# Optimization experiments

Measured on AMD Instinct MI355X. Metric: run time of the kernel, lower is better.

The kernel has to match this reference:

```python
import jax, jax.numpy as jnp
import numpy as np

B, LI, LT, D, H, DH, E, I, IS, TOPK = 2, 1024, 256, 768, 12, 64, 8, 3072, 1536, 2


def _rms(x, s):
    # RMSNorm over last dim, eps=1e-6, learned scale s [DH]
    r = jax.lax.rsqrt(jnp.mean(x * x, axis=-1, keepdims=True) + 1e-6)
    return x * r * s


def _ln(x):
    # LayerNorm without affine (elementwise_affine=False), eps=1e-6
    m = jnp.mean(x, axis=-1, keepdims=True)
    v = jnp.mean((x - m) ** 2, axis=-1, keepdims=True)
    return (x - m) * jax.lax.rsqrt(v + 1e-6)


def _mlp(x, wg, wu, wd):
    # SwiGLU MoeMLP: down(silu(gate(x)) * up(x))
    return (jax.nn.silu(x @ wg.T) * (x @ wu.T)) @ wd.T


def _moe(x, gw, eg, eu, ed, sg, su, sd):
    # x: [T, D]. Softmax gate -> top-k (norm_topk_prob=False -> raw weights),
    # combine expert outputs weighted by routing probs, plus shared experts.
    scores = jax.nn.softmax(x @ gw.T, axis=-1)            # [T, E]
    tw, ti = jax.lax.top_k(scores, TOPK)                  # [T, K]
    T = x.shape[0]
    w = jnp.zeros((T, E), x.dtype).at[jnp.arange(T)[:, None], ti].add(tw)
    y = jnp.zeros_like(x)
    for e in range(E):  # fixed small expert count
        y = y + w[:, e:e + 1] * _mlp(x, eg[e], eu[e], ed[e])
    return y + _mlp(x, sg, su, sd)


def _mod(vec, w, b):
    # Modulation(double=True): Linear(silu(vec)) -> 6 chunks, broadcast over seq
    return jnp.split((jax.nn.silu(vec) @ w.T + b)[:, None, :], 6, axis=-1)


def _qkv(x, w, b, qs, ks):
    Bb, L, _ = x.shape
    qkv = (x @ w.T + b).reshape(Bb, L, 3, H, DH).transpose(2, 0, 3, 1, 4)  # [3,B,H,L,DH]
    q, k, v = qkv[0], qkv[1], qkv[2]
    return _rms(q, qs), _rms(k, ks), v


def _forward(img, txt, vec, imw, imb, tmw, tmb, iqkvw, iqkvb, ipw, ipb, tqkvw, tqkvb, tpw, tpb, iqs, iks, tqs, tks, igw, ieg, ieu, ied, isg, isu, isd, tgw, teg, teu, ted, tsg, tsu, tsd):
    is1, ic1, ig1, is2, ic2, ig2 = _mod(vec, imw, imb)
    ts1, tc1, tg1, ts2, tc2, tg2 = _mod(vec, tmw, tmb)
    iq, ik, iv = _qkv((1 + ic1) * _ln(img) + is1, iqkvw, iqkvb, iqs, iks)
    tq, tk, tv = _qkv((1 + tc1) * _ln(txt) + ts1, tqkvw, tqkvb, tqs, tks)
    # joint attention over concat(txt, img)
    q = jnp.concatenate([tq, iq], axis=2)
    k = jnp.concatenate([tk, ik], axis=2)
    v = jnp.concatenate([tv, iv], axis=2)
    a = jax.nn.softmax(jnp.einsum('bhqd,bhkd->bhqk', q, k) / np.float32(np.sqrt(DH)), axis=-1)
    o = jnp.einsum('bhqk,bhkd->bhqd', a, v).transpose(0, 2, 1, 3).reshape(B, LT + LI, D)
    txt_a, img_a = o[:, :LT], o[:, LT:]
    img = img + ig1 * (img_a @ ipw.T + ipb)
    txt = txt + tg1 * (txt_a @ tpw.T + tpb)
    img = img + ig2 * _moe(((1 + ic2) * _ln(img) + is2).reshape(-1, D), igw, ieg, ieu, ied, isg, isu, isd).reshape(B, LI, D)
    txt = txt + tg2 * _moe(((1 + tc2) * _ln(txt) + ts2).reshape(-1, D), tgw, teg, teu, ted, tsg, tsu, tsd).reshape(B, LT, D)
    return img, txt


def setup_inputs() -> dict:
    key = jax.random.key(0)
    ks = jax.random.split(key, 32)
    n = lambda i, sh, s=1.0: jax.random.normal(ks[i], sh, jnp.float32) * s
    W = 0.02
    return {
        'img': n(0, (B, LI, D)), 'txt': n(1, (B, LT, D)), 'vec': n(2, (B, D)),
        'imw': n(3, (6 * D, D), W), 'imb': n(4, (6 * D,), W),
        'tmw': n(5, (6 * D, D), W), 'tmb': n(6, (6 * D,), W),
        'iqkvw': n(7, (3 * D, D), W), 'iqkvb': n(8, (3 * D,), W),
        'ipw': n(9, (D, D), W), 'ipb': n(10, (D,), W),
        'tqkvw': n(11, (3 * D, D), W), 'tqkvb': n(12, (3 * D,), W),
        'tpw': n(13, (D, D), W), 'tpb': n(14, (D,), W),
        'iqs': jnp.ones((DH,), jnp.float32), 'iks': jnp.ones((DH,), jnp.float32),
        'tqs': jnp.ones((DH,), jnp.float32), 'tks': jnp.ones((DH,), jnp.float32),
        'igw': n(15, (E, D), W), 'ieg': n(16, (E, I, D), W), 'ieu': n(17, (E, I, D), W), 'ied': n(18, (E, D, I), W),
        'isg': n(19, (IS, D), W), 'isu': n(20, (IS, D), W), 'isd': n(21, (D, IS), W),
        'tgw': n(22, (E, D), W), 'teg': n(23, (E, I, D), W), 'teu': n(24, (E, I, D), W), 'ted': n(25, (E, D, I), W),
        'tsg': n(26, (IS, D), W), 'tsu': n(27, (IS, D), W), 'tsd': n(28, (D, IS), W),
    }


def reference(img, txt, vec, imw, imb, tmw, tmb, iqkvw, iqkvb, ipw, ipb, tqkvw, tqkvb, tpw, tpb, iqs, iks, tqs, tks, igw, ieg, ieu, ied, isg, isu, isd, tgw, teg, teu, ted, tsg, tsu, tsd):
    return _forward(img, txt, vec, imw, imb, tmw, tmb, iqkvw, iqkvb, ipw, ipb, tqkvw, tqkvb, tpw, tpb, iqs, iks, tqs, tks, igw, ieg, ieu, ied, isg, isu, isd, tgw, teg, teu, ted, tsg, tsu, tsd)
```

## Files before the change

kernel.cpp:

```cpp
#include <hip/hip_runtime.h>
#include <hip/hip_bf16.h>

using bf16 = __hip_bfloat16;
typedef __attribute__((ext_vector_type(4))) float f32x4;
typedef __attribute__((ext_vector_type(8))) short s16x8;

#define DEV static __device__ __forceinline__
DEV float bf2f(bf16 x){ return __bfloat162float(x); }
DEV bf16  f2bf(float x){ return __float2bfloat16(x); }
DEV float silu_(float x){ return x / (1.f + expf(-x)); }

template<bool B_F32, bool EXPERT, bool GATHER, int OUT, bool BIAS, bool PAIRB, bool MLOOP, bool ABLK>
DEV void gemm_core(
    const bf16* __restrict__ A,
    const void* __restrict__ B0a, const void* __restrict__ B0b,
    const void* __restrict__ B1a, const void* __restrict__ B1b,
    const float* __restrict__ bias, void* __restrict__ C,
    int M, int N, int K, int lda,
    long a_zoff, long b_zoff, int bshift, int biasz, int nsplitB,
    int zdiv, long c_so, long c_si, int ldc,
    float alpha, int ksplit, long c_spo,
    const int* __restrict__ rowlist, const int* __restrict__ offsets,
    const int* __restrict__ counts)
{
  __shared__ __align__(16) char smem_[36864];
  bf16 (*As)[72] = (bf16(*)[72])smem_;
  bf16 (*Bs)[72] = (bf16(*)[72])(smem_ + 18432);
  float (*st)[132] = (float(*)[132])smem_;

  const int zz = blockIdx.z;
  const int n0 = blockIdx.x * 128;
  const int z = zz / ksplit, split = zz % ksplit;
  int Meff = M; long rowbase = 0;
  if (EXPERT){ Meff = counts[z]; rowbase = offsets[z]; }
  int m0 = MLOOP ? 0 : blockIdx.y * 128;
  if (m0 >= Meff) return;
  const bf16* Ab = A + (EXPERT ? 0 : z * a_zoff);
  const int bidx = z >> bshift;
  const long e = (long)(z & ((1 << bshift) - 1));
  const void* BL = bidx ? B1a : B0a;
  const void* BU = bidx ? B1b : B0b;
  long coff;
  if (EXPERT) coff = rowbase * (long)ldc;
  else        coff = (long)(z / zdiv) * c_so + (long)(z % zdiv) * c_si;
  coff += (long)split * c_spo;
  const float* bias_eff = BIAS ? bias + (long)bidx * biasz : nullptr;

  const int klen = K / ksplit;
  const int kbeg = split * klen;
  const int NT = klen >> 6;

  const int tid = threadIdx.x;
  const int lane = tid & 63, wid = tid >> 6;
  const int wm = wid >> 1, wn = wid & 1;
  const int rbase = tid >> 3;
  const int kc = (tid & 7) << 3;

  const bf16* bp[4]; const float* bpf[4];
  bool bvalid[4];
  #pragma unroll
  for (int it = 0; it < 4; it++){
    int br = n0 + rbase + 32 * it;
    bvalid[it] = br < N;
    int brc = bvalid[it] ? br : 0;
    const void* Bsel; long brr;
    if (PAIRB){ Bsel = (brc & 1) ? BU : BL; brr = brc >> 1; }
    else { bool up = brc >= nsplitB; Bsel = up ? BU : BL; brr = up ? (brc - nsplitB) : brc; }
    if (B_F32) bpf[it] = (const float*)Bsel + e * b_zoff + brr * K + kbeg + kc;
    else       bp[it]  = (const bf16*) Bsel + e * b_zoff + brr * K + kbeg + kc;
  }

  const uint4 zero4 = make_uint4(0u,0u,0u,0u);
  const int er = tid >> 3;
  const int ec = (tid & 7) << 4;

  do {
    const bf16* ap[4];
    bool avalid[4];
    #pragma unroll
    for (int it = 0; it < 4; it++){
      int row = rbase + 32 * it;
      long ar = 0;
      if (EXPERT){
        int i = m0 + row;
        avalid[it] = i < Meff;
        if (avalid[it]) ar = GATHER ? (long)rowlist[rowbase + i] : (rowbase + i);
      } else {
        avalid[it] = (m0 + row) < Meff;
        ar = m0 + row;
      }
      if (ABLK) ap[it] = Ab + ((long)(kbeg >> 6) * lda + ar) * 64 + kc;
      else      ap[it] = Ab + ar * (long)lda + kbeg + kc;
    }

    uint4 ra[4], rb[4];
    float4 fb0[4], fb1[4];
    auto LOAD = [&](int koff){
      long aoff = ABLK ? (long)koff * lda : (long)koff;
      #pragma unroll
      for (int it = 0; it < 4; it++){
        ra[it] = avalid[it] ? *(const uint4*)(ap[it] + aoff) : zero4;
        if (B_F32){
          if (bvalid[it]){ fb0[it] = *(const float4*)(bpf[it] + koff);
                           fb1[it] = *(const float4*)(bpf[it] + koff + 4); }
          else { fb0[it] = make_float4(0,0,0,0); fb1[it] = make_float4(0,0,0,0); }
        } else {
          rb[it] = bvalid[it] ? *(const uint4*)(bp[it] + koff) : zero4;
        }
      }
    };
    auto STORE = [&](){
      #pragma unroll
      for (int it = 0; it < 4; it++){
        int row = rbase + 32 * it;
        *(uint4*)(&As[row][kc]) = ra[it];
        if (B_F32){
          union { bf16 h[8]; uint4 v; } u;
          u.h[0]=f2bf(fb0[it].x); u.h[1]=f2bf(fb0[it].y); u.h[2]=f2bf(fb0[it].z); u.h[3]=f2bf(fb0[it].w);
          u.h[4]=f2bf(fb1[it].x); u.h[5]=f2bf(fb1[it].y); u.h[6]=f2bf(fb1[it].z); u.h[7]=f2bf(fb1[it].w);
          *(uint4*)(&Bs[row][kc]) = u.v;
        } else {
          *(uint4*)(&Bs[row][kc]) = rb[it];
        }
      }
    };

    f32x4 acc[4][4] = {};
    LOAD(0);
    for (int t = 0; t < NT; t++){
      STORE();
      __syncthreads();
      if (t + 1 < NT) LOAD((t + 1) << 6);
      #pragma unroll
      for (int ks2 = 0; ks2 < 2; ks2++){
        const int r16 = lane & 15;
        const int kk = ks2 * 32 + ((lane >> 4) << 3);
        s16x8 af[4], bfr[4];
        #pragma unroll
        for (int mi = 0; mi < 4; mi++) af[mi]  = *(const s16x8*)(&As[wm*64 + mi*16 + r16][kk]);
        #pragma unroll
        for (int ni = 0; ni < 4; ni++) bfr[ni] = *(const s16x8*)(&Bs[wn*64 + ni*16 + r16][kk]);
        #pragma unroll
        for (int mi = 0; mi < 4; mi++)
          #pragma unroll
          for (int ni = 0; ni < 4; ni++)
            acc[mi][ni] = __builtin_amdgcn_mfma_f32_16x16x32_bf16(af[mi], bfr[ni], acc[mi][ni], 0, 0, 0);
      }
      __syncthreads();
    }

    const int erg = m0 + (er & 15) + ((er & 16) ? 64 : 0);
    #pragma unroll
    for (int mi = 0; mi < 4; mi++){
      #pragma unroll
      for (int ni = 0; ni < 4; ni++){
        int lc = wn*64 + ni*16 + (lane & 15);
        float bv = 0.f;
        if (BIAS){ if (split == 0) bv = bias_eff[n0 + lc]; }
        #pragma unroll
        for (int i = 0; i < 4; i++){
          int lr = wm*16 + ((lane >> 4) << 2) + i;
          st[lr][lc] = acc[mi][ni][i] * alpha + bv;
        }
      }
      __syncthreads();
      int rg = erg + mi*16;
      if (rg < Meff){
        if (OUT == 3){
          long base = ((long)(n0 >> 7) * (long)ldc + rowbase + rg) * 64 + (ec >> 1);
          union { bf16 h[8]; uint4 v; } o;
          #pragma unroll
          for (int j = 0; j < 8; j++)
            o.h[j] = f2bf(silu_(st[er][ec + 2*j]) * st[er][ec + 2*j + 1]);
          *(uint4*)((bf16*)C + base) = o.v;
        } else {
          int cg = n0 + ec;
          if (cg < N){
            long base = coff + (long)rg * ldc + cg;
            if (OUT == 0){
              float* dst = (float*)C + base;
              #pragma unroll
              for (int q = 0; q < 4; q++)
                *(float4*)(dst + 4*q) = make_float4(st[er][ec+4*q], st[er][ec+4*q+1],
                                                    st[er][ec+4*q+2], st[er][ec+4*q+3]);
            } else {
              union { bf16 h[8]; uint4 v; } o0, o1;
              #pragma unroll
              for (int j = 0; j < 8; j++){
                o0.h[j] = f2bf(st[er][ec+j]);
                o1.h[j] = f2bf(st[er][ec+8+j]);
              }
              *(uint4*)((bf16*)C + base)     = o0.v;
              *(uint4*)((bf16*)C + base + 8) = o1.v;
            }
          }
        }
      }
      __syncthreads();
    }
    m0 += 128;
  } while (MLOOP && m0 < Meff);
}

#define GEMM_K(NAME, BF32, EXPERT, GATHER, OUT, BIAS, PAIRB, MLOOP, ABLK)          \
__global__ __launch_bounds__(256) void NAME(                                       \
    const bf16* A, const void* B0a, const void* B0b, const void* B1a,              \
    const void* B1b, const float* bias, void* C,                                   \
    int M, int N, int K, int lda, long az, long bz, int bshift, int biasz,         \
    int nsplitB, int zdiv, long cso, long csi, int ldc, float alpha, int ks,       \
    long cspo, const int* rl, const int* ofs, const int* cnt){                     \
  gemm_core<BF32,EXPERT,GATHER,OUT,BIAS,PAIRB,MLOOP,ABLK>(A,B0a,B0b,B1a,B1b,bias,C,\
      M,N,K,lda,az,bz,bshift,biasz,nsplitB,zdiv,cso,csi,ldc,alpha,ks,cspo,rl,ofs,cnt); }

GEMM_K(k_qkv,  true ,true ,false,1,true ,false,false,false)
GEMM_K(k_qkt,  false,false,false,1,false,false,false,false)
GEMM_K(k_pv,   false,false,false,0,false,false,false,false)
GEMM_K(k_proj, true ,true ,false,0,true ,false,false,false)
GEMM_K(k_gup,  true ,true ,true ,3,false,true ,true ,false)
GEMM_K(k_down, true ,true ,false,1,false,false,true ,true )
GEMM_K(k_sgup, true ,true ,false,3,false,true ,false,false)
GEMM_K(k_sdown,true ,true ,false,0,false,false,false,true )

__global__ void init_kernel(int* cnt16, int* tabs){
  int i = threadIdx.x;
  if (i < 16) cnt16[i] = 0;
  if (i == 0){
    tabs[0]=2048; tabs[1]=512; tabs[2]=0; tabs[3]=2048;
    tabs[4]=256; tabs[5]=256; tabs[6]=1024; tabs[7]=1024;
    tabs[8]=0; tabs[9]=1280; tabs[10]=256; tabs[11]=1536;
    tabs[12]=2048; tabs[13]=512; tabs[14]=0; tabs[15]=2048;
  }
}
__global__ void tables_kernel(const int* cnt16, int* ofs16, int* cur16){
  if (threadIdx.x == 0){
    int o = 0;
    for (int e = 0; e < 8; e++){ ofs16[e] = o; o += cnt16[e]; cur16[e] = 0; }
    o = 4096;
    for (int e = 8; e < 16; e++){ ofs16[e] = o; o += cnt16[e]; cur16[e] = 0; }
  }
}

__global__ __launch_bounds__(256) void reduce_o_kernel(const float* __restrict__ Op,
    bf16* __restrict__ O, int chunk){
  int zh = blockIdx.y;
  int bh = chunk*12 + zh;
  int b = bh / 12, hh = bh % 12;
  int d = threadIdx.x & 63, rr = threadIdx.x >> 6;
  const float* base = Op + (long)zh * 1280 * 64;
  #pragma unroll
  for (int j = 0; j < 4; j++){
    int row = blockIdx.x * 16 + rr * 4 + j;
    float s = 0.f;
    #pragma unroll
    for (int sp = 0; sp < 5; sp++) s += base[(long)sp*12*1280*64 + (long)row*64 + d];
    O[((long)b*1280 + row)*768 + hh*64 + d] = f2bf(s);
  }
}

__global__ __launch_bounds__(256) void mod_kernel(const float* __restrict__ vec,
    const float* __restrict__ w, const float* __restrict__ b, float* __restrict__ out){
  int bb = blockIdx.y;
  __shared__ float sv[768];
  int tid = threadIdx.x;
  for (int i = tid; i < 768; i += 256){ float v = vec[bb*768 + i]; sv[i] = v/(1.f+expf(-v)); }
  __syncthreads();
  int w4 = tid >> 6, lane = tid & 63;
  int j0 = blockIdx.x * 8 + w4 * 2;
  for (int jj = 0; jj < 2; jj++){
    int j = j0 + jj;
    const float* wr = w + (long)j * 768;
    float p = 0.f;
    #pragma unroll
    for (int i = 0; i < 12; i++) p += sv[lane + 64*i] * wr[lane + 64*i];
    for (int o = 32; o; o >>= 1) p += __shfl_xor(p, o);
    if (lane == 0) out[bb*4608 + j] = p + b[j];
  }
}

__global__ __launch_bounds__(256) void ln_mod_kernel(const float* __restrict__ x,
    const float* __restrict__ mod, bf16* __restrict__ y, int L){
  int t = blockIdx.x; int b = t / L;
  const float* xr = x + (long)t * 768;
  __shared__ float red[256];
  int tid = threadIdx.x;
  float v[3]; float s = 0.f;
  #pragma unroll
  for (int i = 0; i < 3; i++){ v[i] = xr[tid + 256*i]; s += v[i]; }
  red[tid] = s; __syncthreads();
  for (int o = 128; o; o >>= 1){ if (tid < o) red[tid] += red[tid+o]; __syncthreads(); }
  float mean = red[0] * (1.f/768.f); __syncthreads();
  float s2 = 0.f;
  #pragma unroll
  for (int i = 0; i < 3; i++){ float d = v[i]-mean; s2 += d*d; }
  red[tid] = s2; __syncthreads();
  for (int o = 128; o; o >>= 1){ if (tid < o) red[tid] += red[tid+o]; __syncthreads(); }
  float rs = rsqrtf(red[0] * (1.f/768.f) + 1e-6f);
  const float* mb = mod + (long)b * 4608;
  #pragma unroll
  for (int i = 0; i < 3; i++){
    int d = tid + 256*i;
    y[(long)t*768 + d] = f2bf((1.f + mb[768+d]) * ((v[i]-mean)*rs) + mb[d]);
  }
}

__global__ __launch_bounds__(256) void resid_ln_mod_kernel(const float* __restrict__ x,
    const float* __restrict__ pj, int pjoff, long pjspo, const float* __restrict__ mod,
    float* __restrict__ h, bf16* __restrict__ y, float* __restrict__ yf, int L){
  int t = blockIdx.x; int b = t / L;
  const float* mb = mod + (long)b * 4608;
  const float* xr = x + (long)t * 768;
  long pr = (long)(pjoff + b*1280 + (t % L)) * 768;
  __shared__ float red[256];
  int tid = threadIdx.x;
  float v[3]; float s = 0.f;
  #pragma unroll
  for (int i = 0; i < 3; i++){
    int d = tid + 256*i;
    float pv = pj[pr + d] + pj[pjspo + pr + d];
    float hv = xr[d] + mb[2*768 + d] * pv;
    h[(long)t*768 + d] = hv;
    v[i] = hv; s += hv;
  }
  red[tid] = s; __syncthreads();
  for (int o = 128; o; o >>= 1){ if (tid < o) red[tid] += red[tid+o]; __syncthreads(); }
  float mean = red[0] * (1.f/768.f); __syncthreads();
  float s2 = 0.f;
  #pragma unroll
  for (int i = 0; i < 3; i++){ float d = v[i]-mean; s2 += d*d; }
  red[tid] = s2; __syncthreads();
  for (int o = 128; o; o >>= 1){ if (tid < o) red[tid] += red[tid+o]; __syncthreads(); }
  float rs = rsqrtf(red[0] * (1.f/768.f) + 1e-6f);
  #pragma unroll
  for (int i = 0; i < 3; i++){
    int d = tid + 256*i;
    float val = (1.f + mb[4*768+d]) * ((v[i]-mean)*rs) + mb[3*768+d];
    y[(long)t*768 + d] = f2bf(val);
    yf[(long)t*768 + d] = val;
  }
}

__global__ __launch_bounds__(256) void qkv_scatter_kernel(const bf16* __restrict__ qkv,
    const float* __restrict__ qs, const float* __restrict__ ks,
    bf16* __restrict__ Q, bf16* __restrict__ Kb, bf16* __restrict__ Vt,
    int L, int seqoff){
  __shared__ float vt[64][65];
  int bh = blockIdx.y;
  int b = bh / 12, hh = bh % 12;
  int st = blockIdx.x * 64;
  int w = threadIdx.x >> 6, lane = threadIdx.x & 63;
  float qsc = qs[lane], ksc = ks[lane];
  long qkvbase = (long)b * L * 2304;
  long outbase = (long)bh * 1280 * 64;
  #pragma unroll 4
  for (int i = 0; i < 16; i++){
    int r = w*16 + i;
    int t = st + r;
    const bf16* row = qkv + qkvbase + (long)t * 2304;
    float q = bf2f(row[hh*64 + lane]);
    float k = bf2f(row[768 + hh*64 + lane]);
    float v = bf2f(row[1536 + hh*64 + lane]);
    float q2 = q*q, k2 = k*k;
    for (int o = 32; o; o >>= 1){ q2 += __shfl_xor(q2, o); k2 += __shfl_xor(k2, o); }
    q = q * rsqrtf(q2*(1.f/64.f) + 1e-6f) * qsc;
    k = k * rsqrtf(k2*(1.f/64.f) + 1e-6f) * ksc;
    int seq = seqoff + t;
    Q [outbase + (long)seq*64 + lane] = f2bf(q);
    Kb[outbase + (long)seq*64 + lane] = f2bf(k);
    vt[r][lane] = v;
  }
  __syncthreads();
  #pragma unroll 4
  for (int i = 0; i < 16; i++){
    int d = w*16 + i;
    Vt[outbase + (long)d*1280 + seqoff + st + lane] = f2bf(vt[lane][d]);
  }
}

__global__ __launch_bounds__(256) void softmax_kernel(const bf16* __restrict__ S, bf16* __restrict__ P){
  long r = blockIdx.x;
  const bf16* sr = S + r * 1280;
  __shared__ float buf[1280];
  __shared__ float red[256];
  int tid = threadIdx.x;
  float mx = -1e30f;
  for (int i = tid; i < 1280; i += 256){ float v = bf2f(sr[i]); buf[i] = v; mx = fmaxf(mx, v); }
  red[tid] = mx; __syncthreads();
  for (int o = 128; o; o >>= 1){ if (tid < o) red[tid] = fmaxf(red[tid], red[tid+o]); __syncthreads(); }
  float m = red[0]; __syncthreads();
  float s = 0.f;
  for (int i = tid; i < 1280; i += 256){ float e = expf(buf[i] - m); buf[i] = e; s += e; }
  red[tid] = s; __syncthreads();
  for (int o = 128; o; o >>= 1){ if (tid < o) red[tid] += red[tid+o]; __syncthreads(); }
  float inv = 1.f / red[0];
  bf16* pr = P + r * 1280;
  for (int i = tid; i < 1280; i += 256) pr[i] = f2bf(buf[i] * inv);
}

__global__ __launch_bounds__(256) void router_kernel(const float* __restrict__ x2,
    const float* __restrict__ gw, float* __restrict__ tkw, int* __restrict__ tki,
    int* __restrict__ counts, int T){
  int t = blockIdx.x * 4 + (threadIdx.x >> 6);
  int lane = threadIdx.x & 63;
  if (t >= T) return;
  const float* xr = x2 + (long)t * 768;
  float xs[12];
  #pragma unroll
  for (int i = 0; i < 12; i++) xs[i] = xr[lane + 64*i];
  float sc[8];
  #pragma unroll
  for (int e = 0; e < 8; e++){
    const float* gr = gw + e * 768;
    float p = 0.f;
    #pragma unroll
    for (int i = 0; i < 12; i++) p += xs[i] * gr[lane + 64*i];
    for (int o = 32; o; o >>= 1) p += __shfl_xor(p, o);
    sc[e] = p;
  }
  if (lane == 0){
    float m = sc[0];
    for (int e = 1; e < 8; e++) m = fmaxf(m, sc[e]);
    float s = 0.f;
    for (int e = 0; e < 8; e++){ sc[e] = expf(sc[e] - m); s += sc[e]; }
    float inv = 1.f / s;
    for (int e = 0; e < 8; e++) sc[e] *= inv;
    int i0 = 0;
    for (int e = 1; e < 8; e++) if (sc[e] > sc[i0]) i0 = e;
    int i1 = -1;
    for (int e = 0; e < 8; e++){ if (e == i0) continue; if (i1 < 0 || sc[e] > sc[i1]) i1 = e; }
    tkw[t*2] = sc[i0]; tkw[t*2+1] = sc[i1];
    tki[t*2] = i0;     tki[t*2+1] = i1;
    atomicAdd(&counts[i0], 1); atomicAdd(&counts[i1], 1);
  }
}

__global__ __launch_bounds__(256) void scatter_kernel(const int* __restrict__ tki,
    const int* __restrict__ ofs16, int* __restrict__ cur16,
    int* __restrict__ rows16, int* __restrict__ tpos, int T, int tabofs, int rowadd){
  int idx = blockIdx.x * 256 + threadIdx.x;
  if (idx >= T * 2) return;
  int t = idx >> 1;
  int e = tki[idx];
  int pos = atomicAdd(&cur16[tabofs + e], 1);
  int g = ofs16[tabofs + e] + pos;
  rows16[g] = rowadd + t;
  tpos[idx] = g;
}

__global__ __launch_bounds__(256) void combine_kernel(const float* __restrict__ h,
    const float* __restrict__ mod, const float* __restrict__ tkw, const int* __restrict__ tpos,
    const bf16* __restrict__ ye, long espo, const float* __restrict__ ys, long sspo,
    float* __restrict__ out, int L){
  int t = blockIdx.x; int b = t / L;
  const float* g2 = mod + (long)b * 4608 + 5*768;
  float w0 = tkw[t*2], w1 = tkw[t*2+1];
  long p0 = (long)tpos[t*2] * 768, p1 = (long)tpos[t*2+1] * 768;
  for (int d = threadIdx.x; d < 768; d += 256){
    float e0 = 0.f, e1 = 0.f, sv = 0.f;
    #pragma unroll
    for (int sp = 0; sp < 8; sp++){
      e0 += bf2f(ye[sp*espo + p0 + d]);
      e1 += bf2f(ye[sp*espo + p1 + d]);
    }
    #pragma unroll
    for (int sp = 0; sp < 2; sp++) sv += ys[sp*sspo + (long)t*768 + d];
    out[(long)t*768 + d] = h[(long)t*768 + d] + g2[d] * (w0*e0 + w1*e1 + sv);
  }
}

extern "C" void kernel_launch(void* const* d_in, const int* in_sizes, int n_in,
                              void* d_out, int out_size, void* d_ws, size_t ws_size,
                              hipStream_t stream){
  (void)in_sizes; (void)n_in; (void)out_size; (void)ws_size;
  const float* fin[33];
  for (int i = 0; i < 33; i++) fin[i] = (const float*)d_in[i];
  float* out_img = (float*)d_out;
  float* out_txt = (float*)d_out + (long)2*1024*768;

  char* ws = (char*)d_ws;
  size_t off = 0;
  auto alloc = [&](size_t n)->char*{
    off = (off + 255) & ~(size_t)255;
    char* p = ws + off; off += n; return p;
  };

  float* mod_i=(float*)alloc(2*4608*4);
  float* mod_t=(float*)alloc(2*4608*4);
  float* h_i  =(float*)alloc((size_t)2048*768*4);
  float* h_t  =(float*)alloc((size_t)512*768*4);
  bf16*  x2c  =(bf16*) alloc((size_t)2560*768*2);
  float* x2fc =(float*)alloc((size_t)2560*768*4);
  float* tkw_i=(float*)alloc(2048*2*4);
  int*   tki_i=(int*)  alloc(2048*2*4);
  float* tkw_t=(float*)alloc(512*2*4);
  int*   tki_t=(int*)  alloc(512*2*4);
  int* cnt16=(int*)alloc(16*4);
  int* ofs16=(int*)alloc(16*4);
  int* cur16=(int*)alloc(16*4);
  int* rows16=(int*)alloc(5120*4);
  int* tpos_i=(int*)alloc(4096*4);
  int* tpos_t=(int*)alloc(1024*4);
  int* tabs=(int*)alloc(64*4);
  float* qb_ws=(float*)alloc(2*2304*4);
  float* pb_ws=(float*)alloc(2*768*4);

  size_t arena = (off + 255) & ~(size_t)255;
  off = arena;
  bf16* Qb=(bf16*)alloc((size_t)24*1280*64*2);
  bf16* Kb=(bf16*)alloc((size_t)24*1280*64*2);
  bf16* Vt=(bf16*)alloc((size_t)24*1280*64*2);
  bf16* O =(bf16*)alloc((size_t)2*1280*768*2);
  float* pjc=(float*)alloc((size_t)2*2560*768*4);
  size_t sub = (off + 255) & ~(size_t)255;
  bf16* xmc=(bf16*)alloc((size_t)2560*768*2);
  bf16* qrc=(bf16*)alloc((size_t)2560*2304*2);
  off = sub;
  bf16* S=(bf16*)alloc((size_t)12*1280*1280*2);
  float* Opart=(float*)alloc((size_t)5*12*1280*64*4);
  off = arena;
  bf16*  h1 =(bf16*) alloc((size_t)48*5120*64*2);
  bf16*  ye =(bf16*) alloc((size_t)8*5120*768*2);
  bf16*  h1s=(bf16*) alloc((size_t)24*2560*64*2);
  float* ys =(float*)alloc((size_t)2*2560*768*4);

  hipMemcpyAsync(qb_ws,      fin[8],  2304*4, hipMemcpyDeviceToDevice, stream);
  hipMemcpyAsync(qb_ws+2304, fin[12], 2304*4, hipMemcpyDeviceToDevice, stream);
  hipMemcpyAsync(pb_ws,      fin[14], 768*4,  hipMemcpyDeviceToDevice, stream);
  hipMemcpyAsync(pb_ws+768,  fin[10], 768*4,  hipMemcpyDeviceToDevice, stream);

  init_kernel<<<1, 64, 0, stream>>>(cnt16, tabs);
  mod_kernel<<<dim3(576,2), 256, 0, stream>>>(fin[2], fin[3], fin[4], mod_i);
  mod_kernel<<<dim3(576,2), 256, 0, stream>>>(fin[2], fin[5], fin[6], mod_t);
  ln_mod_kernel<<<2048, 256, 0, stream>>>(fin[0], mod_i, xmc, 1024);
  ln_mod_kernel<<<512,  256, 0, stream>>>(fin[1], mod_t, xmc + (long)2048*768, 256);

  k_qkv<<<dim3(18,16,2), 256, 0, stream>>>(xmc, fin[7], fin[7], fin[11], fin[11],
      qb_ws, qrc, 0, 2304, 768, 768, 0, 0, 0, 2304, 2304,
      1, 0, 0, 2304, 1.f, 1, 0, nullptr, tabs+2, tabs+0);
  qkv_scatter_kernel<<<dim3(16,24), 256, 0, stream>>>(qrc, fin[15], fin[16], Qb, Kb, Vt, 1024, 256);
  qkv_scatter_kernel<<<dim3(4,24),  256, 0, stream>>>(qrc + (long)2048*2304, fin[17], fin[18], Qb, Kb, Vt, 256, 0);

  for (int ch = 0; ch < 2; ch++){
    const bf16* Qc = Qb + (size_t)ch * 12 * 1280 * 64;
    const bf16* Kc = Kb + (size_t)ch * 12 * 1280 * 64;
    const bf16* Vc = Vt + (size_t)ch * 12 * 1280 * 64;
    k_qkt<<<dim3(10,10,12), 256, 0, stream>>>(Qc, Kc, Kc, Kc, Kc, nullptr, S,
        1280, 1280, 64, 64, (long)1280*64, (long)1280*64, 30, 0, 1280,
        1, (long)1280*1280, 0, 1280, 0.125f, 1, 0, nullptr, nullptr, nullptr);
    softmax_kernel<<<12*1280, 256, 0, stream>>>(S, S);
    k_pv<<<dim3(1,10,60), 256, 0, stream>>>(S, Vc, Vc, Vc, Vc, nullptr, Opart,
        1280, 64, 1280, 1280, (long)1280*1280, (long)64*1280, 30, 0, 64,
        1, (long)1280*64, 0, 64, 1.f, 5, (long)12*1280*64, nullptr, nullptr, nullptr);
    reduce_o_kernel<<<dim3(80,12), 256, 0, stream>>>(Opart, O, ch);
  }

  k_proj<<<dim3(6,8,8), 256, 0, stream>>>(O, fin[13], fin[13], fin[9], fin[9],
      pb_ws, pjc, 0, 768, 768, 768, 0, 0, 1, 768, 768,
      1, 0, 0, 768, 1.f, 2, (long)2560*768, nullptr, tabs+8, tabs+4);
  resid_ln_mod_kernel<<<2048, 256, 0, stream>>>(fin[0], pjc, 256, (long)2560*768,
      mod_i, h_i, x2c, x2fc, 1024);
  resid_ln_mod_kernel<<<512, 256, 0, stream>>>(fin[1], pjc, 0, (long)2560*768,
      mod_t, h_t, x2c + (long)2048*768, x2fc + (long)2048*768, 256);

  router_kernel<<<512, 256, 0, stream>>>(x2fc, fin[19], tkw_i, tki_i, cnt16, 2048);
  router_kernel<<<128, 256, 0, stream>>>(x2fc + (long)2048*768, fin[26], tkw_t, tki_t, cnt16+8, 512);
  tables_kernel<<<1, 1, 0, stream>>>(cnt16, ofs16, cur16);
  scatter_kernel<<<16, 256, 0, stream>>>(tki_i, ofs16, cur16, rows16, tpos_i, 2048, 0, 0);
  scatter_kernel<<<4,  256, 0, stream>>>(tki_t, ofs16, cur16, rows16, tpos_t, 512, 8, 2048);

  k_gup<<<dim3(48,1,16), 256, 0, stream>>>(x2c, fin[20], fin[21], fin[27], fin[28],
      nullptr, h1, 0, 6144, 768, 768, 0, (long)3072*768, 3, 0, 0,
      1, 0, 0, 5120, 1.f, 1, 0, rows16, ofs16, cnt16);
  k_down<<<dim3(6,1,128), 256, 0, stream>>>(h1, fin[22], fin[22], fin[29], fin[29],
      nullptr, ye, 0, 768, 3072, 5120, 0, (long)768*3072, 3, 0, 768,
      1, 0, 0, 768, 1.f, 8, (long)5120*768, nullptr, ofs16, cnt16);
  k_sgup<<<dim3(24,16,2), 256, 0, stream>>>(x2c, fin[23], fin[24], fin[30], fin[31],
      nullptr, h1s, 0, 3072, 768, 768, 0, 0, 0, 0, 0,
      1, 0, 0, 2560, 1.f, 1, 0, nullptr, tabs+14, tabs+12);
  k_sdown<<<dim3(6,16,4), 256, 0, stream>>>(h1s, fin[25], fin[25], fin[32], fin[32],
      nullptr, ys, 0, 768, 1536, 2560, 0, 0, 0, 0, 768,
      1, 0, 0, 768, 1.f, 2, (long)2560*768, nullptr, tabs+14, tabs+12);

  combine_kernel<<<2048, 256, 0, stream>>>(h_i, mod_i, tkw_i, tpos_i,
      ye, (long)5120*768, ys, (long)2560*768, out_img, 1024);
  combine_kernel<<<512, 256, 0, stream>>>(h_t, mod_t, tkw_t, tpos_t,
      ye, (long)5120*768, ys + (long)2048*768, (long)2560*768, out_txt, 256);
}
```

Measured before the change: 1.080 ms.

## Parallelize expert GEMMs over M-tiles and merge attention chunks into one launch

The expert gate/up and down GEMMs no longer have each block loop over all M-tiles of an expert. They launch a grid with 16 M-tiles in y, and blocks past an expert's row count exit early. The two 12-head attention chunks are merged into single QK^T, softmax, PV and reduce launches over 24 heads, which doubles the score and partial-output scratch buffers. This adds parallelism and cuts launch and tail overhead, at the cost of many empty blocks and more workspace memory.

```diff
diff --git a/kernel.cpp b/kernel.cpp
--- a/kernel.cpp
+++ b/kernel.cpp
@@ -10,7 +10,7 @@
 DEV bf16  f2bf(float x){ return __float2bfloat16(x); }
 DEV float silu_(float x){ return x / (1.f + expf(-x)); }
 
-template<bool B_F32, bool EXPERT, bool GATHER, int OUT, bool BIAS, bool PAIRB, bool MLOOP, bool ABLK>
+template<bool B_F32, bool EXPERT, bool GATHER, int OUT, bool BIAS, bool PAIRB, bool ABLK>
 DEV void gemm_core(
     const bf16* __restrict__ A,
     const void* __restrict__ B0a, const void* __restrict__ B0b,
@@ -33,7 +33,7 @@
   const int z = zz / ksplit, split = zz % ksplit;
   int Meff = M; long rowbase = 0;
   if (EXPERT){ Meff = counts[z]; rowbase = offsets[z]; }
-  int m0 = MLOOP ? 0 : blockIdx.y * 128;
+  const int m0 = blockIdx.y * 128;
   if (m0 >= Meff) return;
   const bf16* Ab = A + (EXPERT ? 0 : z * a_zoff);
   const int bidx = z >> bshift;
@@ -69,157 +69,153 @@
     if (B_F32) bpf[it] = (const float*)Bsel + e * b_zoff + brr * K + kbeg + kc;
     else       bp[it]  = (const bf16*) Bsel + e * b_zoff + brr * K + kbeg + kc;
   }
+  const bf16* ap[4];
+  bool avalid[4];
+  #pragma unroll
+  for (int it = 0; it < 4; it++){
+    int row = rbase + 32 * it;
+    long ar = 0;
+    if (EXPERT){
+      int i = m0 + row;
+      avalid[it] = i < Meff;
+      if (avalid[it]) ar = GATHER ? (long)rowlist[rowbase + i] : (rowbase + i);
+    } else {
+      avalid[it] = (m0 + row) < Meff;
+      ar = m0 + row;
+    }
+    if (ABLK) ap[it] = Ab + ((long)(kbeg >> 6) * lda + ar) * 64 + kc;
+    else      ap[it] = Ab + ar * (long)lda + kbeg + kc;
+  }
 
   const uint4 zero4 = make_uint4(0u,0u,0u,0u);
+  uint4 ra[4], rb[4];
+  float4 fb0[4], fb1[4];
+
+  auto LOAD = [&](int koff){
+    long aoff = ABLK ? (long)koff * lda : (long)koff;
+    #pragma unroll
+    for (int it = 0; it < 4; it++){
+      ra[it] = avalid[it] ? *(const uint4*)(ap[it] + aoff) : zero4;
+      if (B_F32){
+        if (bvalid[it]){ fb0[it] = *(const float4*)(bpf[it] + koff);
+                         fb1[it] = *(const float4*)(bpf[it] + koff + 4); }
+        else { fb0[it] = make_float4(0,0,0,0); fb1[it] = make_float4(0,0,0,0); }
+      } else {
+        rb[it] = bvalid[it] ? *(const uint4*)(bp[it] + koff) : zero4;
+      }
+    }
+  };
+  auto STORE = [&](){
+    #pragma unroll
+    for (int it = 0; it < 4; it++){
+      int row = rbase + 32 * it;
+      *(uint4*)(&As[row][kc]) = ra[it];
+      if (B_F32){
+        union { bf16 h[8]; uint4 v; } u;
+        u.h[0]=f2bf(fb0[it].x); u.h[1]=f2bf(fb0[it].y); u.h[2]=f2bf(fb0[it].z); u.h[3]=f2bf(fb0[it].w);
+        u.h[4]=f2bf(fb1[it].x); u.h[5]=f2bf(fb1[it].y); u.h[6]=f2bf(fb1[it].z); u.h[7]=f2bf(fb1[it].w);
+        *(uint4*)(&Bs[row][kc]) = u.v;
+      } else {
+        *(uint4*)(&Bs[row][kc]) = rb[it];
+      }
+    }
+  };
+
+  f32x4 acc[4][4] = {};
+  LOAD(0);
+  for (int t = 0; t < NT; t++){
+    STORE();
+    __syncthreads();
+    if (t + 1 < NT) LOAD((t + 1) << 6);
+    #pragma unroll
+    for (int ks2 = 0; ks2 < 2; ks2++){
+      const int r16 = lane & 15;
+      const int kk = ks2 * 32 + ((lane >> 4) << 3);
+      s16x8 af[4], bfr[4];
+      #pragma unroll
+      for (int mi = 0; mi < 4; mi++) af[mi]  = *(const s16x8*)(&As[wm*64 + mi*16 + r16][kk]);
+      #pragma unroll
+      for (int ni = 0; ni < 4; ni++) bfr[ni] = *(const s16x8*)(&Bs[wn*64 + ni*16 + r16][kk]);
+      #pragma unroll
+      for (int mi = 0; mi < 4; mi++)
+        #pragma unroll
+        for (int ni = 0; ni < 4; ni++)
+          acc[mi][ni] = __builtin_amdgcn_mfma_f32_16x16x32_bf16(af[mi], bfr[ni], acc[mi][ni], 0, 0, 0);
+    }
+    __syncthreads();
+  }
+
   const int er = tid >> 3;
   const int ec = (tid & 7) << 4;
-
-  do {
-    const bf16* ap[4];
-    bool avalid[4];
-    #pragma unroll
-    for (int it = 0; it < 4; it++){
-      int row = rbase + 32 * it;
-      long ar = 0;
-      if (EXPERT){
-        int i = m0 + row;
-        avalid[it] = i < Meff;
-        if (avalid[it]) ar = GATHER ? (long)rowlist[rowbase + i] : (rowbase + i);
+  const int erg = m0 + (er & 15) + ((er & 16) ? 64 : 0);
+  #pragma unroll
+  for (int mi = 0; mi < 4; mi++){
+    #pragma unroll
+    for (int ni = 0; ni < 4; ni++){
+      int lc = wn*64 + ni*16 + (lane & 15);
+      float bv = 0.f;
+      if (BIAS){ if (split == 0) bv = bias_eff[n0 + lc]; }
+      #pragma unroll
+      for (int i = 0; i < 4; i++){
+        int lr = wm*16 + ((lane >> 4) << 2) + i;
+        st[lr][lc] = acc[mi][ni][i] * alpha + bv;
+      }
+    }
+    __syncthreads();
+    int rg = erg + mi*16;
+    if (rg < Meff){
+      if (OUT == 3){
+        long base = ((long)(n0 >> 7) * (long)ldc + rowbase + rg) * 64 + (ec >> 1);
+        union { bf16 h[8]; uint4 v; } o;
+        #pragma unroll
+        for (int j = 0; j < 8; j++)
+          o.h[j] = f2bf(silu_(st[er][ec + 2*j]) * st[er][ec + 2*j + 1]);
+        *(uint4*)((bf16*)C + base) = o.v;
       } else {
-        avalid[it] = (m0 + row) < Meff;
-        ar = m0 + row;
-      }
-      if (ABLK) ap[it] = Ab + ((long)(kbeg >> 6) * lda + ar) * 64 + kc;
-      else      ap[it] = Ab + ar * (long)lda + kbeg + kc;
-    }
-
-    uint4 ra[4], rb[4];
-    float4 fb0[4], fb1[4];
-    auto LOAD = [&](int koff){
-      long aoff = ABLK ? (long)koff * lda : (long)koff;
-      #pragma unroll
-      for (int it = 0; it < 4; it++){
-        ra[it] = avalid[it] ? *(const uint4*)(ap[it] + aoff) : zero4;
-        if (B_F32){
-          if (bvalid[it]){ fb0[it] = *(const float4*)(bpf[it] + koff);
-                           fb1[it] = *(const float4*)(bpf[it] + koff + 4); }
-          else { fb0[it] = make_float4(0,0,0,0); fb1[it] = make_float4(0,0,0,0); }
-        } else {
-          rb[it] = bvalid[it] ? *(const uint4*)(bp[it] + koff) : zero4;
-        }
-      }
-    };
-    auto STORE = [&](){
-      #pragma unroll
-      for (int it = 0; it < 4; it++){
-        int row = rbase + 32 * it;
-        *(uint4*)(&As[row][kc]) = ra[it];
-        if (B_F32){
-          union { bf16 h[8]; uint4 v; } u;
-          u.h[0]=f2bf(fb0[it].x); u.h[1]=f2bf(fb0[it].y); u.h[2]=f2bf(fb0[it].z); u.h[3]=f2bf(fb0[it].w);
-          u.h[4]=f2bf(fb1[it].x); u.h[5]=f2bf(fb1[it].y); u.h[6]=f2bf(fb1[it].z); u.h[7]=f2bf(fb1[it].w);
-          *(uint4*)(&Bs[row][kc]) = u.v;
-        } else {
-          *(uint4*)(&Bs[row][kc]) = rb[it];
-        }
-      }
-    };
-
-    f32x4 acc[4][4] = {};
-    LOAD(0);
-    for (int t = 0; t < NT; t++){
-      STORE();
-      __syncthreads();
-      if (t + 1 < NT) LOAD((t + 1) << 6);
-      #pragma unroll
-      for (int ks2 = 0; ks2 < 2; ks2++){
-        const int r16 = lane & 15;
-        const int kk = ks2 * 32 + ((lane >> 4) << 3);
-        s16x8 af[4], bfr[4];
-        #pragma unroll
-        for (int mi = 0; mi < 4; mi++) af[mi]  = *(const s16x8*)(&As[wm*64 + mi*16 + r16][kk]);
-        #pragma unroll
-        for (int ni = 0; ni < 4; ni++) bfr[ni] = *(const s16x8*)(&Bs[wn*64 + ni*16 + r16][kk]);
-        #pragma unroll
-        for (int mi = 0; mi < 4; mi++)
-          #pragma unroll
-          for (int ni = 0; ni < 4; ni++)
-            acc[mi][ni] = __builtin_amdgcn_mfma_f32_16x16x32_bf16(af[mi], bfr[ni], acc[mi][ni], 0, 0, 0);
-      }
-      __syncthreads();
-    }
-
-    const int erg = m0 + (er & 15) + ((er & 16) ? 64 : 0);
-    #pragma unroll
-    for (int mi = 0; mi < 4; mi++){
-      #pragma unroll
-      for (int ni = 0; ni < 4; ni++){
-        int lc = wn*64 + ni*16 + (lane & 15);
-        float bv = 0.f;
-        if (BIAS){ if (split == 0) bv = bias_eff[n0 + lc]; }
-        #pragma unroll
-        for (int i = 0; i < 4; i++){
-          int lr = wm*16 + ((lane >> 4) << 2) + i;
-          st[lr][lc] = acc[mi][ni][i] * alpha + bv;
-        }
-      }
-      __syncthreads();
-      int rg = erg + mi*16;
-      if (rg < Meff){
-        if (OUT == 3){
-          long base = ((long)(n0 >> 7) * (long)ldc + rowbase + rg) * 64 + (ec >> 1);
-          union { bf16 h[8]; uint4 v; } o;
-          #pragma unroll
-          for (int j = 0; j < 8; j++)
-            o.h[j] = f2bf(silu_(st[er][ec + 2*j]) * st[er][ec + 2*j + 1]);
-          *(uint4*)((bf16*)C + base) = o.v;
-        } else {
-          int cg = n0 + ec;
-          if (cg < N){
-            long base = coff + (long)rg * ldc + cg;
-            if (OUT == 0){
-              float* dst = (float*)C + base;
-              #pragma unroll
-              for (int q = 0; q < 4; q++)
-                *(float4*)(dst + 4*q) = make_float4(st[er][ec+4*q], st[er][ec+4*q+1],
-                                                    st[er][ec+4*q+2], st[er][ec+4*q+3]);
-            } else {
-              union { bf16 h[8]; uint4 v; } o0, o1;
-              #pragma unroll
-              for (int j = 0; j < 8; j++){
-                o0.h[j] = f2bf(st[er][ec+j]);
-                o1.h[j] = f2bf(st[er][ec+8+j]);
-              }
-              *(uint4*)((bf16*)C + base)     = o0.v;
-              *(uint4*)((bf16*)C + base + 8) = o1.v;
+        int cg = n0 + ec;
+        if (cg < N){
+          long base = coff + (long)rg * ldc + cg;
+          if (OUT == 0){
+            float* dst = (float*)C + base;
+            #pragma unroll
+            for (int q = 0; q < 4; q++)
+              *(float4*)(dst + 4*q) = make_float4(st[er][ec+4*q], st[er][ec+4*q+1],
+                                                  st[er][ec+4*q+2], st[er][ec+4*q+3]);
+          } else {
+            union { bf16 h[8]; uint4 v; } o0, o1;
+            #pragma unroll
+            for (int j = 0; j < 8; j++){
+              o0.h[j] = f2bf(st[er][ec+j]);
+              o1.h[j] = f2bf(st[er][ec+8+j]);
             }
+            *(uint4*)((bf16*)C + base)     = o0.v;
+            *(uint4*)((bf16*)C + base + 8) = o1.v;
           }
         }
       }
-      __syncthreads();
-    }
-    m0 += 128;
-  } while (MLOOP && m0 < Meff);
-}
-
-#define GEMM_K(NAME, BF32, EXPERT, GATHER, OUT, BIAS, PAIRB, MLOOP, ABLK)          \
+    }
+    __syncthreads();
+  }
+}
+
+#define GEMM_K(NAME, BF32, EXPERT, GATHER, OUT, BIAS, PAIRB, ABLK)                 \
 __global__ __launch_bounds__(256) void NAME(                                       \
     const bf16* A, const void* B0a, const void* B0b, const void* B1a,              \
     const void* B1b, const float* bias, void* C,                                   \
     int M, int N, int K, int lda, long az, long bz, int bshift, int biasz,         \
     int nsplitB, int zdiv, long cso, long csi, int ldc, float alpha, int ks,       \
     long cspo, const int* rl, const int* ofs, const int* cnt){                     \
-  gemm_core<BF32,EXPERT,GATHER,OUT,BIAS,PAIRB,MLOOP,ABLK>(A,B0a,B0b,B1a,B1b,bias,C,\
+  gemm_core<BF32,EXPERT,GATHER,OUT,BIAS,PAIRB,ABLK>(A,B0a,B0b,B1a,B1b,bias,C,      \
       M,N,K,lda,az,bz,bshift,biasz,nsplitB,zdiv,cso,csi,ldc,alpha,ks,cspo,rl,ofs,cnt); }
 
-GEMM_K(k_qkv,  true ,true ,false,1,true ,false,false,false)
-GEMM_K(k_qkt,  false,false,false,1,false,false,false,false)
-GEMM_K(k_pv,   false,false,false,0,false,false,false,false)
-GEMM_K(k_proj, true ,true ,false,0,true ,false,false,false)
-GEMM_K(k_gup,  true ,true ,true ,3,false,true ,true ,false)
-GEMM_K(k_down, true ,true ,false,1,false,false,true ,true )
-GEMM_K(k_sgup, true ,true ,false,3,false,true ,false,false)
-GEMM_K(k_sdown,true ,true ,false,0,false,false,false,true )
+GEMM_K(k_qkv,  true ,true ,false,1,true ,false,false)
+GEMM_K(k_qkt,  false,false,false,1,false,false,false)
+GEMM_K(k_pv,   false,false,false,0,false,false,false)
+GEMM_K(k_proj, true ,true ,false,0,true ,false,false)
+GEMM_K(k_gup,  true ,true ,true ,3,false,true ,false)
+GEMM_K(k_down, true ,true ,false,1,false,false,true )
+GEMM_K(k_sgup, true ,true ,false,3,false,true ,false)
+GEMM_K(k_sdown,true ,true ,false,0,false,false,true )
 
 __global__ void init_kernel(int* cnt16, int* tabs){
   int i = threadIdx.x;
@@ -241,18 +237,17 @@
 }
 
 __global__ __launch_bounds__(256) void reduce_o_kernel(const float* __restrict__ Op,
-    bf16* __restrict__ O, int chunk){
-  int zh = blockIdx.y;
-  int bh = chunk*12 + zh;
+    bf16* __restrict__ O, int nh){
+  int bh = blockIdx.y;
   int b = bh / 12, hh = bh % 12;
   int d = threadIdx.x & 63, rr = threadIdx.x >> 6;
-  const float* base = Op + (long)zh * 1280 * 64;
+  const float* base = Op + (long)bh * 1280 * 64;
   #pragma unroll
   for (int j = 0; j < 4; j++){
     int row = blockIdx.x * 16 + rr * 4 + j;
     float s = 0.f;
     #pragma unroll
-    for (int sp = 0; sp < 5; sp++) s += base[(long)sp*12*1280*64 + (long)row*64 + d];
+    for (int sp = 0; sp < 5; sp++) s += base[(long)sp*nh*1280*64 + (long)row*64 + d];
     O[((long)b*1280 + row)*768 + hh*64 + d] = f2bf(s);
   }
 }
@@ -514,8 +509,8 @@
   bf16* xmc=(bf16*)alloc((size_t)2560*768*2);
   bf16* qrc=(bf16*)alloc((size_t)2560*2304*2);
   off = sub;
-  bf16* S=(bf16*)alloc((size_t)12*1280*1280*2);
-  float* Opart=(float*)alloc((size_t)5*12*1280*64*4);
+  bf16* S=(bf16*)alloc((size_t)24*1280*1280*2);
+  float* Opart=(float*)alloc((size_t)5*24*1280*64*4);
   off = arena;
   bf16*  h1 =(bf16*) alloc((size_t)48*5120*64*2);
   bf16*  ye =(bf16*) alloc((size_t)8*5120*768*2);
@@ -539,19 +534,14 @@
   qkv_scatter_kernel<<<dim3(16,24), 256, 0, stream>>>(qrc, fin[15], fin[16], Qb, Kb, Vt, 1024, 256);
   qkv_scatter_kernel<<<dim3(4,24),  256, 0, stream>>>(qrc + (long)2048*2304, fin[17], fin[18], Qb, Kb, Vt, 256, 0);
 
-  for (int ch = 0; ch < 2; ch++){
-    const bf16* Qc = Qb + (size_t)ch * 12 * 1280 * 64;
-    const bf16* Kc = Kb + (size_t)ch * 12 * 1280 * 64;
-    const bf16* Vc = Vt + (size_t)ch * 12 * 1280 * 64;
-    k_qkt<<<dim3(10,10,12), 256, 0, stream>>>(Qc, Kc, Kc, Kc, Kc, nullptr, S,
-        1280, 1280, 64, 64, (long)1280*64, (long)1280*64, 30, 0, 1280,
-        1, (long)1280*1280, 0, 1280, 0.125f, 1, 0, nullptr, nullptr, nullptr);
-    softmax_kernel<<<12*1280, 256, 0, stream>>>(S, S);
-    k_pv<<<dim3(1,10,60), 256, 0, stream>>>(S, Vc, Vc, Vc, Vc, nullptr, Opart,
-        1280, 64, 1280, 1280, (long)1280*1280, (long)64*1280, 30, 0, 64,
-        1, (long)1280*64, 0, 64, 1.f, 5, (long)12*1280*64, nullptr, nullptr, nullptr);
-    reduce_o_kernel<<<dim3(80,12), 256, 0, stream>>>(Opart, O, ch);
-  }
+  k_qkt<<<dim3(10,10,24), 256, 0, stream>>>(Qb, Kb, Kb, Kb, Kb, nullptr, S,
+      1280, 1280, 64, 64, (long)1280*64, (long)1280*64, 30, 0, 1280,
+      1, (long)1280*1280, 0, 1280, 0.125f, 1, 0, nullptr, nullptr, nullptr);
+  softmax_kernel<<<24*1280, 256, 0, stream>>>(S, S);
+  k_pv<<<dim3(1,10,120), 256, 0, stream>>>(S, Vt, Vt, Vt, Vt, nullptr, Opart,
+      1280, 64, 1280, 1280, (long)1280*1280, (long)64*1280, 30, 0, 64,
+      1, (long)1280*64, 0, 64, 1.f, 5, (long)24*1280*64, nullptr, nullptr, nullptr);
+  reduce_o_kernel<<<dim3(80,24), 256, 0, stream>>>(Opart, O, 24);
 
   k_proj<<<dim3(6,8,8), 256, 0, stream>>>(O, fin[13], fin[13], fin[9], fin[9],
       pb_ws, pjc, 0, 768, 768, 768, 0, 0, 1, 768, 768,
@@ -567,10 +557,10 @@
   scatter_kernel<<<16, 256, 0, stream>>>(tki_i, ofs16, cur16, rows16, tpos_i, 2048, 0, 0);
   scatter_kernel<<<4,  256, 0, stream>>>(tki_t, ofs16, cur16, rows16, tpos_t, 512, 8, 2048);
 
-  k_gup<<<dim3(48,1,16), 256, 0, stream>>>(x2c, fin[20], fin[21], fin[27], fin[28],
+  k_gup<<<dim3(48,16,16), 256, 0, stream>>>(x2c, fin[20], fin[21], fin[27], fin[28],
       nullptr, h1, 0, 6144, 768, 768, 0, (long)3072*768, 3, 0, 0,
       1, 0, 0, 5120, 1.f, 1, 0, rows16, ofs16, cnt16);
-  k_down<<<dim3(6,1,128), 256, 0, stream>>>(h1, fin[22], fin[22], fin[29], fin[29],
+  k_down<<<dim3(6,16,128), 256, 0, stream>>>(h1, fin[22], fin[22], fin[29], fin[29],
       nullptr, ye, 0, 768, 3072, 5120, 0, (long)768*3072, 3, 0, 768,
       1, 0, 0, 768, 1.f, 8, (long)5120*768, nullptr, ofs16, cnt16);
   k_sgup<<<dim3(24,16,2), 256, 0, stream>>>(x2c, fin[23], fin[24], fin[30], fin[31],
```

Measured after the change: 1.091 ms. No clear change (+1.0%).
